# Optimization experiments

Measured on AMD Instinct MI355X. Metric: run time of the kernel, lower is better.

The kernel has to match this reference:

```python
import jax, jax.numpy as jnp
import numpy as np

D_MODEL = 1024
N_HEADS = 16
HEAD_DIM = D_MODEL // N_HEADS


def setup_inputs() -> dict:
    key = jax.random.key(0)
    ks = jax.random.split(key, 5)
    scale = 1.0 / np.sqrt(D_MODEL)
    x = jax.random.normal(ks[0], (2, 2048, D_MODEL), dtype=jnp.float32)
    Wq = jax.random.normal(ks[1], (D_MODEL, D_MODEL), dtype=jnp.float32) * scale
    Wk = jax.random.normal(ks[2], (D_MODEL, D_MODEL), dtype=jnp.float32) * scale
    Wv = jax.random.normal(ks[3], (D_MODEL, D_MODEL), dtype=jnp.float32) * scale
    Wo = jax.random.normal(ks[4], (D_MODEL, D_MODEL), dtype=jnp.float32) * scale
    return {"x": x, "Wq": Wq, "Wk": Wk, "Wv": Wv, "Wo": Wo}


def reference(x, Wq, Wk, Wv, Wo):
    # x: [B, S, D]; weights stored as [out, in] like nn.Linear -> y = x @ W.T
    B, S, D = x.shape
    H, Hd = N_HEADS, HEAD_DIM
    attn_scale = 1.0 / np.sqrt(Hd)

    def split_heads(t):  # [B,S,D] -> [B,H,S,Hd]
        return t.reshape(B, S, H, Hd).transpose(0, 2, 1, 3)

    q = split_heads(x @ Wq.T)
    k = split_heads(x @ Wk.T)
    v = split_heads(x @ Wv.T)

    scores = jnp.einsum('bhqd,bhkd->bhqk', q, k) * attn_scale  # [B,H,S,S]
    causal = jnp.tril(jnp.ones((S, S), dtype=bool))
    scores = jnp.where(causal, scores, jnp.finfo(scores.dtype).min)
    attn = jax.nn.softmax(scores, axis=-1)
    out = jnp.einsum('bhqk,bhkd->bhqd', attn, v)  # [B,H,S,Hd]
    out = out.transpose(0, 2, 1, 3).reshape(B, S, D)
    return out @ Wo.T
```

## Files before the change

### kernel.cpp

```cpp
#include <hip/hip_runtime.h>
#include <hip/hip_bf16.h>

typedef __attribute__((ext_vector_type(8))) __bf16 bf16x8;
typedef __attribute__((ext_vector_type(4))) __bf16 bf16x4;
typedef __attribute__((ext_vector_type(4))) float f32x4;

#define D_MODEL 1024
#define S_LEN   2048
#define BATCH   2
#define NH      16
#define HD      64
#define MROWS   (BATCH * S_LEN)

#define EXP2F(x) __builtin_amdgcn_exp2f(x)

__global__ __launch_bounds__(256) void cvt_bf16(const float* __restrict__ in,
                                                __bf16* __restrict__ out, int n4) {
    int i = blockIdx.x * 256 + threadIdx.x;
    if (i < n4) {
        float4 v = ((const float4*)in)[i];
        bf16x4 o = {(__bf16)v.x, (__bf16)v.y, (__bf16)v.z, (__bf16)v.w};
        ((bf16x4*)out)[i] = o;
    }
}

__global__ __launch_bounds__(256) void cvt_all(const float* __restrict__ x,
                                               const float* __restrict__ Wq,
                                               const float* __restrict__ Wk,
                                               const float* __restrict__ Wv,
                                               __bf16* __restrict__ xb,
                                               __bf16* __restrict__ wqkv) {
    const int nx = (MROWS * D_MODEL) / 4;
    const int nw = (D_MODEL * D_MODEL) / 4;
    int i = blockIdx.x * 256 + threadIdx.x;
    const float* src;
    __bf16* dst;
    int si, di;
    if (i < nx) {
        src = x; si = i; dst = xb; di = i;
    } else {
        int k = i - nx;
        int sel = k / nw;
        si = k - sel * nw;
        src = (sel == 0) ? Wq : (sel == 1) ? Wk : Wv;
        dst = wqkv; di = k;
    }
    float4 v = ((const float4*)src)[si];
    bf16x4 o = {(__bf16)v.x, (__bf16)v.y, (__bf16)v.z, (__bf16)v.w};
    ((bf16x4*)dst)[di] = o;
}

__device__ __forceinline__ void g2l16(const void* g, __bf16* l) {
    __builtin_amdgcn_global_load_lds((const __attribute__((address_space(1))) void*)g,
                                     (__attribute__((address_space(3))) void*)l, 16, 0, 0);
}

__global__ __launch_bounds__(256) void gemm_qkv(const __bf16* __restrict__ A,
                                                const __bf16* __restrict__ W,
                                                __bf16* __restrict__ Qb,
                                                __bf16* __restrict__ Kq,
                                                __bf16* __restrict__ VTb,
                                                float qs) {
    __shared__ __bf16 sa[128 * 64];
    __shared__ __bf16 sb[128 * 64];

    const int t    = threadIdx.x;
    const int lane = t & 63;
    const int wid  = t >> 6;
    const int lr   = lane & 15;
    const int lg   = lane >> 4;
    const int wr   = wid >> 1;
    const int wc   = wid & 1;
    const int K    = D_MODEL;

    const int bid  = blockIdx.x;
    const int swz  = (bid & 7) * 96 + (bid >> 3);
    const int m0   = (swz / 24) * 128;
    const int n0   = (swz % 24) * 128;

    const __bf16* Ab = A + (size_t)m0 * K;
    const __bf16* Wb = W + (size_t)n0 * K;

    f32x4 acc[4][4];
#pragma unroll
    for (int m = 0; m < 4; m++)
#pragma unroll
        for (int n = 0; n < 4; n++) acc[m][n] = (f32x4){0.f, 0.f, 0.f, 0.f};

    for (int k0 = 0; k0 < K; k0 += 64) {
#pragma unroll
        for (int i = 0; i < 4; i++) {
            int ca = i * 256 + t;
            int row = ca >> 3;
            int sc  = ((ca & 7) ^ (row & 7)) * 8;
            g2l16(&Ab[(size_t)row * K + k0 + sc], &sa[ca * 8]);
            g2l16(&Wb[(size_t)row * K + k0 + sc], &sb[ca * 8]);
        }
        __syncthreads();

        bf16x8 af[4][2], bfr[4][2];
#pragma unroll
        for (int m = 0; m < 4; m++) {
            const int row = wr * 64 + m * 16 + lr;
#pragma unroll
            for (int kc = 0; kc < 2; kc++)
                af[m][kc] = *(const bf16x8*)&sa[row * 64 + (((kc * 4 + lg) ^ (lr & 7)) * 8)];
        }
#pragma unroll
        for (int n = 0; n < 4; n++) {
            const int row = wc * 64 + n * 16 + lr;
#pragma unroll
            for (int kc = 0; kc < 2; kc++)
                bfr[n][kc] = *(const bf16x8*)&sb[row * 64 + (((kc * 4 + lg) ^ (lr & 7)) * 8)];
        }
#pragma unroll
        for (int m = 0; m < 4; m++)
#pragma unroll
            for (int n = 0; n < 4; n++)
#pragma unroll
                for (int kc = 0; kc < 2; kc++)
                    acc[m][n] = __builtin_amdgcn_mfma_f32_16x16x32_bf16(af[m][kc], bfr[n][kc], acc[m][n], 0, 0, 0);
        __syncthreads();
    }

#pragma unroll
    for (int m = 0; m < 4; m++) {
#pragma unroll
        for (int n = 0; n < 4; n++) {
#pragma unroll
            for (int j = 0; j < 4; j++) {
                int row = m0 + wr * 64 + m * 16 + lg * 4 + j;
                int col = n0 + wc * 64 + n * 16 + lr;
                float v = acc[m][n][j];
                if (col < 1024) {
                    Qb[(size_t)row * D_MODEL + col] = (__bf16)(v * qs);
                } else if (col < 2048) {
                    Kq[(size_t)row * D_MODEL + col - 1024] = (__bf16)v;
                } else {
                    int c2 = col - 2048;
                    int b = row >> 11, s = row & 2047;
                    int h = c2 >> 6, d = c2 & 63;
                    VTb[(((size_t)(b * NH + h) * HD + d) << 11) + s] = (__bf16)v;
                }
            }
        }
    }
}

__global__ __launch_bounds__(256) void gemm_out(const __bf16* __restrict__ A,
                                                const __bf16* __restrict__ W,
                                                float* __restrict__ C,
                                                int M, int N, int K) {
    __shared__ __bf16 sa[128 * 64];
    __shared__ __bf16 sb[64 * 64];

    const int t    = threadIdx.x;
    const int lane = t & 63;
    const int wid  = t >> 6;
    const int lr   = lane & 15;
    const int lg   = lane >> 4;
    const int wr   = wid >> 1;
    const int wc   = wid & 1;

    const int bid  = blockIdx.x;
    const int swz  = (bid & 7) * 64 + (bid >> 3);
    const int m0   = (swz / 16) * 128;
    const int n0   = (swz % 16) * 64;

    const __bf16* Ab = A + (size_t)m0 * K;
    const __bf16* Wb = W + (size_t)n0 * K;

    f32x4 acc[4][2];
#pragma unroll
    for (int m = 0; m < 4; m++)
#pragma unroll
        for (int n = 0; n < 2; n++) acc[m][n] = (f32x4){0.f, 0.f, 0.f, 0.f};

    for (int k0 = 0; k0 < K; k0 += 64) {
#pragma unroll
        for (int i = 0; i < 4; i++) {
            int ca = i * 256 + t;
            int row = ca >> 3;
            int sc  = ((ca & 7) ^ (row & 7)) * 8;
            g2l16(&Ab[(size_t)row * K + k0 + sc], &sa[ca * 8]);
        }
#pragma unroll
        for (int i = 0; i < 2; i++) {
            int ca = i * 256 + t;
            int row = ca >> 3;
            int sc  = ((ca & 7) ^ (row & 7)) * 8;
            g2l16(&Wb[(size_t)row * K + k0 + sc], &sb[ca * 8]);
        }
        __syncthreads();

        bf16x8 af[4][2], bfr[2][2];
#pragma unroll
        for (int m = 0; m < 4; m++) {
            const int row = wr * 64 + m * 16 + lr;
#pragma unroll
            for (int kc = 0; kc < 2; kc++)
                af[m][kc] = *(const bf16x8*)&sa[row * 64 + (((kc * 4 + lg) ^ (lr & 7)) * 8)];
        }
#pragma unroll
        for (int n = 0; n < 2; n++) {
            const int row = wc * 32 + n * 16 + lr;
#pragma unroll
            for (int kc = 0; kc < 2; kc++)
                bfr[n][kc] = *(const bf16x8*)&sb[row * 64 + (((kc * 4 + lg) ^ (lr & 7)) * 8)];
        }
#pragma unroll
        for (int m = 0; m < 4; m++)
#pragma unroll
            for (int n = 0; n < 2; n++)
#pragma unroll
                for (int kc = 0; kc < 2; kc++)
                    acc[m][n] = __builtin_amdgcn_mfma_f32_16x16x32_bf16(af[m][kc], bfr[n][kc], acc[m][n], 0, 0, 0);
        __syncthreads();
    }

#pragma unroll
    for (int m = 0; m < 4; m++)
#pragma unroll
        for (int n = 0; n < 2; n++)
#pragma unroll
            for (int j = 0; j < 4; j++) {
                int row = m0 + wr * 64 + m * 16 + lg * 4 + j;
                int col = n0 + wc * 32 + n * 16 + lr;
                C[(size_t)row * N + col] = acc[m][n][j];
            }
}

__global__ __launch_bounds__(512) void attn_fwd(const __bf16* __restrict__ Q,
                                                const __bf16* __restrict__ Kb,
                                                const __bf16* __restrict__ VT,
                                                __bf16* __restrict__ O) {
    __shared__ __bf16 kt[2][64 * 64];
    __shared__ __bf16 vt[2][64 * 64];
    __shared__ __bf16 pt[8][16][64];

    const int t    = threadIdx.x;
    const int lane = t & 63;
    const int wid  = t >> 6;
    const int lr   = lane & 15;
    const int lg   = lane >> 4;
    const int bid  = blockIdx.x;
    const int qb   = 15 - (bid >> 5);
    const int bh   = bid & 31;
    const int b    = bh >> 4;
    const int h    = bh & 15;
    const int col  = h * HD;

    const size_t qrow = (size_t)b * S_LEN + qb * 128 + wid * 16;
    const int qg = qb * 128 + wid * 16 + lr;
    const __bf16* Kbase = Kb + (size_t)b * S_LEN * D_MODEL + col;
    const __bf16* Vbase = VT + (size_t)bh * HD * S_LEN;
    const int pswz = (lr & 7) * 8;

    const int ca0 = t;
    const int r0 = ca0 >> 3, s0 = ((ca0 & 7) ^ (r0 & 7)) * 8;

    bf16x8 qf[2];
#pragma unroll
    for (int c = 0; c < 2; c++)
        qf[c] = *(const bf16x8*)&Q[(qrow + lr) * D_MODEL + col + c * 32 + lg * 8];

    f32x4 o[4];
#pragma unroll
    for (int n = 0; n < 4; n++) o[n] = (f32x4){0.f, 0.f, 0.f, 0.f};
    float psum = 0.f;

    const int nkv = 2 * qb + 2;

    g2l16(&Kbase[(size_t)r0 * D_MODEL + s0], &kt[0][ca0 * 8]);
    g2l16(&Vbase[(size_t)r0 * S_LEN + s0],   &vt[0][ca0 * 8]);

    for (int kvt = 0; kvt < nkv; kvt++) {
        const int kv0 = kvt * 64;
        const int cur = kvt & 1;
        const int nb  = cur ^ 1;

        {
            const int kvn = (kvt + 1 < nkv) ? kvt + 1 : nkv - 1;
            const int kv1 = kvn * 64;
            g2l16(&Kbase[(size_t)(kv1 + r0) * D_MODEL + s0], &kt[nb][ca0 * 8]);
            g2l16(&Vbase[(size_t)r0 * S_LEN + kv1 + s0],     &vt[nb][ca0 * 8]);
        }

        asm volatile("s_waitcnt vmcnt(2)" ::: "memory");
        __builtin_amdgcn_sched_barrier(0);
        __builtin_amdgcn_s_barrier();
        __builtin_amdgcn_sched_barrier(0);

        f32x4 s[4];
        __builtin_amdgcn_s_setprio(1);
#pragma unroll
        for (int tt = 0; tt < 4; tt++) {
            s[tt] = (f32x4){0.f, 0.f, 0.f, 0.f};
#pragma unroll
            for (int c = 0; c < 2; c++) {
                const int row = tt * 16 + lr;
                bf16x8 kf = *(const bf16x8*)&kt[cur][row * 64 + (((c * 4 + lg) ^ (lr & 7)) * 8)];
                s[tt] = __builtin_amdgcn_mfma_f32_16x16x32_bf16(kf, qf[c], s[tt], 0, 0, 0);
            }
        }
        __builtin_amdgcn_s_setprio(0);

        if (kv0 + 63 > qg) {
#pragma unroll
            for (int tt = 0; tt < 4; tt++) {
                int kg = kv0 + tt * 16 + lg * 4;
#pragma unroll
                for (int j = 0; j < 4; j++)
                    if (kg + j > qg) s[tt][j] = -1e30f;
            }
        }

#pragma unroll
        for (int tt = 0; tt < 4; tt++) {
            float p0 = EXP2F(s[tt][0]), p1 = EXP2F(s[tt][1]);
            float p2 = EXP2F(s[tt][2]), p3 = EXP2F(s[tt][3]);
            psum += (p0 + p1) + (p2 + p3);
            bf16x4 pw = {(__bf16)p0, (__bf16)p1, (__bf16)p2, (__bf16)p3};
            *(bf16x4*)&pt[wid][lr][(tt * 16 + lg * 4) ^ pswz] = pw;
        }

        asm volatile("s_waitcnt lgkmcnt(0)" ::: "memory");
        __builtin_amdgcn_sched_barrier(0);

        __builtin_amdgcn_s_setprio(1);
#pragma unroll
        for (int c = 0; c < 2; c++) {
            bf16x8 pa = *(const bf16x8*)&pt[wid][lr][(c * 32 + lg * 8) ^ pswz];
#pragma unroll
            for (int n = 0; n < 4; n++) {
                const int d = n * 16 + lr;
                bf16x8 vf = *(const bf16x8*)&vt[cur][d * 64 + (((c * 4 + lg) ^ (lr & 7)) * 8)];
                o[n] = __builtin_amdgcn_mfma_f32_16x16x32_bf16(pa, vf, o[n], 0, 0, 0);
            }
        }
        __builtin_amdgcn_s_setprio(0);

        __builtin_amdgcn_sched_barrier(0);
        __builtin_amdgcn_s_barrier();
        __builtin_amdgcn_sched_barrier(0);
    }

    psum += __shfl_xor(psum, 16, 64);
    psum += __shfl_xor(psum, 32, 64);
    float inv = 1.0f / psum;
    float invj[4];
#pragma unroll
    for (int j = 0; j < 4; j++) invj[j] = __shfl(inv, lg * 4 + j, 64);

#pragma unroll
    for (int n = 0; n < 4; n++) {
#pragma unroll
        for (int j = 0; j < 4; j++) {
            float val = o[n][j] * invj[j];
            O[(qrow + lg * 4 + j) * D_MODEL + col + n * 16 + lr] = (__bf16)val;
        }
    }
}

extern "C" void kernel_launch(void* const* d_in, const int* in_sizes, int n_in,
                              void* d_out, int out_size, void* d_ws, size_t ws_size,
                              hipStream_t stream) {
    const float* x  = (const float*)d_in[0];
    const float* Wq = (const float*)d_in[1];
    const float* Wk = (const float*)d_in[2];
    const float* Wv = (const float*)d_in[3];
    const float* Wo = (const float*)d_in[4];
    float* out = (float*)d_out;

    const size_t XE = (size_t)MROWS * D_MODEL;
    const size_t WE = (size_t)D_MODEL * D_MODEL;
    __bf16* xb  = (__bf16*)d_ws;
    __bf16* Qb  = xb + XE;
    __bf16* Kq  = Qb + XE;
    __bf16* VTb = Kq + XE;
    __bf16* AO  = xb;

    __bf16* wqkv = (__bf16*)d_out;
    __bf16* wob  = Qb;

    const int ncv = (int)(XE / 4 + 3 * WE / 4);
    cvt_all<<<(ncv + 255) / 256, 256, 0, stream>>>(x, Wq, Wk, Wv, xb, wqkv);

    const float qs = 0.125f * 1.44269504088896340736f;
    gemm_qkv<<<768, 256, 0, stream>>>(xb, wqkv, Qb, Kq, VTb, qs);

    attn_fwd<<<512, 512, 0, stream>>>(Qb, Kq, VTb, AO);

    cvt_bf16<<<(int)(WE / 4 / 256), 256, 0, stream>>>(Wo, wob, (int)(WE / 4));
    gemm_out<<<512, 256, 0, stream>>>(AO, wob, out, MROWS, D_MODEL, D_MODEL);
}
```

Measured before the change: 112.8 us.

## Double-buffer LDS tiles in QKV and output GEMMs with async prefetch

Both projection GEMMs now keep two LDS buffers for the A and W tiles. Each iteration issues the global-to-LDS loads for the next K tile before computing on the current one, and waits with an explicit vmcnt so only the current tile's loads must have landed. This is meant to hide global load latency behind the MFMA work. In exchange, LDS use per block doubles, which may lower occupancy. On the last iteration a redundant tile is loaded into the unused buffer.

```diff
diff --git a/kernel.cpp b/kernel.cpp
--- a/kernel.cpp
+++ b/kernel.cpp
@@ -61,8 +61,8 @@
                                                 __bf16* __restrict__ Kq,
                                                 __bf16* __restrict__ VTb,
                                                 float qs) {
-    __shared__ __bf16 sa[128 * 64];
-    __shared__ __bf16 sb[128 * 64];
+    __shared__ __bf16 sa[2][128 * 64];
+    __shared__ __bf16 sb[2][128 * 64];
 
     const int t    = threadIdx.x;
     const int lane = t & 63;
@@ -87,16 +87,29 @@
 #pragma unroll
         for (int n = 0; n < 4; n++) acc[m][n] = (f32x4){0.f, 0.f, 0.f, 0.f};
 
-    for (int k0 = 0; k0 < K; k0 += 64) {
+    auto stage = [&](int buf, int k0) {
 #pragma unroll
         for (int i = 0; i < 4; i++) {
             int ca = i * 256 + t;
             int row = ca >> 3;
             int sc  = ((ca & 7) ^ (row & 7)) * 8;
-            g2l16(&Ab[(size_t)row * K + k0 + sc], &sa[ca * 8]);
-            g2l16(&Wb[(size_t)row * K + k0 + sc], &sb[ca * 8]);
-        }
-        __syncthreads();
+            g2l16(&Ab[(size_t)row * K + k0 + sc], &sa[buf][ca * 8]);
+            g2l16(&Wb[(size_t)row * K + k0 + sc], &sb[buf][ca * 8]);
+        }
+    };
+
+    stage(0, 0);
+
+    for (int k0 = 0; k0 < K; k0 += 64) {
+        const int cur = (k0 >> 6) & 1;
+        const int nb  = cur ^ 1;
+        const int kn  = (k0 + 64 < K) ? k0 + 64 : k0;
+        stage(nb, kn);
+
+        asm volatile("s_waitcnt vmcnt(8)" ::: "memory");
+        __builtin_amdgcn_sched_barrier(0);
+        __builtin_amdgcn_s_barrier();
+        __builtin_amdgcn_sched_barrier(0);
 
         bf16x8 af[4][2], bfr[4][2];
 #pragma unroll
@@ -104,14 +117,14 @@
             const int row = wr * 64 + m * 16 + lr;
 #pragma unroll
             for (int kc = 0; kc < 2; kc++)
-                af[m][kc] = *(const bf16x8*)&sa[row * 64 + (((kc * 4 + lg) ^ (lr & 7)) * 8)];
+                af[m][kc] = *(const bf16x8*)&sa[cur][row * 64 + (((kc * 4 + lg) ^ (lr & 7)) * 8)];
         }
 #pragma unroll
         for (int n = 0; n < 4; n++) {
             const int row = wc * 64 + n * 16 + lr;
 #pragma unroll
             for (int kc = 0; kc < 2; kc++)
-                bfr[n][kc] = *(const bf16x8*)&sb[row * 64 + (((kc * 4 + lg) ^ (lr & 7)) * 8)];
+                bfr[n][kc] = *(const bf16x8*)&sb[cur][row * 64 + (((kc * 4 + lg) ^ (lr & 7)) * 8)];
         }
 #pragma unroll
         for (int m = 0; m < 4; m++)
@@ -120,7 +133,10 @@
 #pragma unroll
                 for (int kc = 0; kc < 2; kc++)
                     acc[m][n] = __builtin_amdgcn_mfma_f32_16x16x32_bf16(af[m][kc], bfr[n][kc], acc[m][n], 0, 0, 0);
-        __syncthreads();
+
+        __builtin_amdgcn_sched_barrier(0);
+        __builtin_amdgcn_s_barrier();
+        __builtin_amdgcn_sched_barrier(0);
     }
 
 #pragma unroll
@@ -151,8 +167,8 @@
                                                 const __bf16* __restrict__ W,
                                                 float* __restrict__ C,
                                                 int M, int N, int K) {
-    __shared__ __bf16 sa[128 * 64];
-    __shared__ __bf16 sb[64 * 64];
+    __shared__ __bf16 sa[2][128 * 64];
+    __shared__ __bf16 sb[2][64 * 64];
 
     const int t    = threadIdx.x;
     const int lane = t & 63;
@@ -176,22 +192,35 @@
 #pragma unroll
         for (int n = 0; n < 2; n++) acc[m][n] = (f32x4){0.f, 0.f, 0.f, 0.f};
 
-    for (int k0 = 0; k0 < K; k0 += 64) {
+    auto stage = [&](int buf, int k0) {
 #pragma unroll
         for (int i = 0; i < 4; i++) {
             int ca = i * 256 + t;
             int row = ca >> 3;
             int sc  = ((ca & 7) ^ (row & 7)) * 8;
-            g2l16(&Ab[(size_t)row * K + k0 + sc], &sa[ca * 8]);
+            g2l16(&Ab[(size_t)row * K + k0 + sc], &sa[buf][ca * 8]);
         }
 #pragma unroll
         for (int i = 0; i < 2; i++) {
             int ca = i * 256 + t;
             int row = ca >> 3;
             int sc  = ((ca & 7) ^ (row & 7)) * 8;
-            g2l16(&Wb[(size_t)row * K + k0 + sc], &sb[ca * 8]);
-        }
-        __syncthreads();
+            g2l16(&Wb[(size_t)row * K + k0 + sc], &sb[buf][ca * 8]);
+        }
+    };
+
+    stage(0, 0);
+
+    for (int k0 = 0; k0 < K; k0 += 64) {
+        const int cur = (k0 >> 6) & 1;
+        const int nb  = cur ^ 1;
+        const int kn  = (k0 + 64 < K) ? k0 + 64 : k0;
+        stage(nb, kn);
+
+        asm volatile("s_waitcnt vmcnt(6)" ::: "memory");
+        __builtin_amdgcn_sched_barrier(0);
+        __builtin_amdgcn_s_barrier();
+        __builtin_amdgcn_sched_barrier(0);
 
         bf16x8 af[4][2], bfr[2][2];
 #pragma unroll
@@ -199,14 +228,14 @@
             const int row = wr * 64 + m * 16 + lr;
 #pragma unroll
             for (int kc = 0; kc < 2; kc++)
-                af[m][kc] = *(const bf16x8*)&sa[row * 64 + (((kc * 4 + lg) ^ (lr & 7)) * 8)];
+                af[m][kc] = *(const bf16x8*)&sa[cur][row * 64 + (((kc * 4 + lg) ^ (lr & 7)) * 8)];
         }
 #pragma unroll
         for (int n = 0; n < 2; n++) {
             const int row = wc * 32 + n * 16 + lr;
 #pragma unroll
             for (int kc = 0; kc < 2; kc++)
-                bfr[n][kc] = *(const bf16x8*)&sb[row * 64 + (((kc * 4 + lg) ^ (lr & 7)) * 8)];
+                bfr[n][kc] = *(const bf16x8*)&sb[cur][row * 64 + (((kc * 4 + lg) ^ (lr & 7)) * 8)];
         }
 #pragma unroll
         for (int m = 0; m < 4; m++)
@@ -215,7 +244,10 @@
 #pragma unroll
                 for (int kc = 0; kc < 2; kc++)
                     acc[m][n] = __builtin_amdgcn_mfma_f32_16x16x32_bf16(af[m][kc], bfr[n][kc], acc[m][n], 0, 0, 0);
-        __syncthreads();
+
+        __builtin_amdgcn_sched_barrier(0);
+        __builtin_amdgcn_s_barrier();
+        __builtin_amdgcn_sched_barrier(0);
     }
 
 #pragma unroll
```

Result: slower. 131.4 us (+16.5%).
